# Performance work log

Measured on AMD Instinct MI355X. Metric: run time of the kernel, lower is better.

Reference implementation:

```python
import jax, jax.numpy as jnp
import numpy as np

NUM_QUANTIZERS = 8  # num_quantizes in __init__


def l2norm(t, eps=1e-12):
    return t / jnp.clip(jnp.linalg.norm(t, axis=-1, keepdims=True), eps)


def setup_inputs() -> dict:
    key = jax.random.key(0)
    k1, k2 = jax.random.split(key)
    x = jax.random.normal(k1, (1, 16384, 512), dtype=jnp.float32)
    codebook = jax.random.normal(k2, (2048, 512), dtype=jnp.float32)
    return {"x": x, "codebook": codebook}


def reference(x, codebook):
    # cosine-sim codebook: codes live on the unit sphere
    cb = l2norm(codebook)  # [K, D]

    def step(residual, _):
        rn = l2norm(residual)                       # [1, S, D]
        sim = jnp.einsum('bsd,kd->bsk', rn, cb)     # [1, S, K]
        idx = jnp.argmax(sim, axis=-1)              # [1, S]
        q = cb[idx]                                 # [1, S, D] gather
        # commit loss: mse(quantize.detach(), input)
        commit = jnp.mean((jax.lax.stop_gradient(q) - residual) ** 2)
        # straight-through estimator
        q_st = residual + jax.lax.stop_gradient(q - residual)
        return residual - q_st, (q_st, idx, commit)

    _, (quantized, indices, commits) = jax.lax.scan(
        step, x, None, length=NUM_QUANTIZERS)
    # quantized: [n, 1, S, D]; sum over quantizer axis (keepdim batch=1)
    quantized_sum = jnp.sum(quantized, axis=0)      # [1, S, D]
    all_indices = jnp.transpose(indices, (1, 2, 0))  # [1, S, n]
    commit_losses = commits[None, :]                # [1, n]
    return quantized_sum, all_indices, commit_losses
```

## Files before the change

### kernel.cpp

```cpp
#include <hip/hip_runtime.h>
#include <math.h>


#define TOKENS 16384
#define DDIM   512
#define NCODE  2048
#define NQ     8
#define CHUNK  4096

#define CBN_OFF  0u
#define G_OFF    1048576u
#define S_OFF    5242880u
#define ACC_FULL (S_OFF + (size_t)TOKENS * NCODE)
#define ACC_CHNK (S_OFF + (size_t)CHUNK  * NCODE)

#define QS_OFF   0u
#define IDX_OFF  8388608u
#define CL_OFF   8519680u

__global__ __launch_bounds__(256) void normalize_cb(const float* __restrict__ cb,
                                                    float* __restrict__ cbn,
                                                    float* __restrict__ acc) {
  if (blockIdx.x == 0 && threadIdx.x < NQ) acc[threadIdx.x] = 0.0f;
  int lane = threadIdx.x & 63;
  int wv   = threadIdx.x >> 6;
  int row  = blockIdx.x * 4 + wv;
  const float4* rp = (const float4*)(cb + (size_t)row * DDIM);
  float4 a = rp[lane * 2 + 0];
  float4 b = rp[lane * 2 + 1];
  float ss = a.x*a.x + a.y*a.y + a.z*a.z + a.w*a.w
           + b.x*b.x + b.y*b.y + b.z*b.z + b.w*b.w;
  #pragma unroll
  for (int o = 1; o < 64; o <<= 1) ss += __shfl_xor(ss, o);
  float nrm = fmaxf(sqrtf(ss), 1e-12f);
  float4 o0 = make_float4(a.x/nrm, a.y/nrm, a.z/nrm, a.w/nrm);
  float4 o1 = make_float4(b.x/nrm, b.y/nrm, b.z/nrm, b.w/nrm);
  float4* op = (float4*)(cbn + (size_t)row * DDIM);
  op[lane * 2 + 0] = o0;
  op[lane * 2 + 1] = o1;
}

__global__ void finalize(const float* __restrict__ acc, float* __restrict__ out) {
  if (threadIdx.x < NQ)
    out[CL_OFF + threadIdx.x] = acc[threadIdx.x] * (1.0f / ((float)TOKENS * (float)DDIM));
}

__global__ __launch_bounds__(256) void gemm_nt(const float* __restrict__ A,
                                               const float* __restrict__ B,
                                               float* __restrict__ C) {
  const int K = DDIM, N = NCODE;
  __shared__ float As[2][16][132];
  __shared__ float Bs[2][16][132];
  const int bn = blockIdx.x * 128;
  const int bm = blockIdx.y * 128;
  const int t  = threadIdx.x;
  const int tx = t & 15;
  const int ty = t >> 4;
  const int lr = t >> 2;
  const int lc = (t & 3) * 4;

  float acc[8][8];
  #pragma unroll
  for (int i = 0; i < 8; ++i)
    #pragma unroll
    for (int j = 0; j < 8; ++j) acc[i][j] = 0.0f;

  const float* Ap = A + (size_t)(bm + lr) * K + lc;
  const float* Bp = B + (size_t)(bn + lr) * K + lc;

  float4 a0 = *(const float4*)(Ap);
  float4 a1 = *(const float4*)(Ap + (size_t)64 * K);
  float4 b0 = *(const float4*)(Bp);
  float4 b1 = *(const float4*)(Bp + (size_t)64 * K);

  int cur = 0;
  for (int k0 = 0; k0 < K; k0 += 16) {
    As[cur][lc+0][lr]    = a0.x; As[cur][lc+1][lr]    = a0.y;
    As[cur][lc+2][lr]    = a0.z; As[cur][lc+3][lr]    = a0.w;
    As[cur][lc+0][lr+64] = a1.x; As[cur][lc+1][lr+64] = a1.y;
    As[cur][lc+2][lr+64] = a1.z; As[cur][lc+3][lr+64] = a1.w;
    Bs[cur][lc+0][lr]    = b0.x; Bs[cur][lc+1][lr]    = b0.y;
    Bs[cur][lc+2][lr]    = b0.z; Bs[cur][lc+3][lr]    = b0.w;
    Bs[cur][lc+0][lr+64] = b1.x; Bs[cur][lc+1][lr+64] = b1.y;
    Bs[cur][lc+2][lr+64] = b1.z; Bs[cur][lc+3][lr+64] = b1.w;
    if (k0 + 16 < K) {
      a0 = *(const float4*)(Ap + k0 + 16);
      a1 = *(const float4*)(Ap + (size_t)64 * K + k0 + 16);
      b0 = *(const float4*)(Bp + k0 + 16);
      b1 = *(const float4*)(Bp + (size_t)64 * K + k0 + 16);
    }
    __syncthreads();
    #pragma unroll
    for (int kk = 0; kk < 16; ++kk) {
      float av[8], bv[8];
      *(float4*)(av + 0) = *(const float4*)&As[cur][kk][ty * 4];
      *(float4*)(av + 4) = *(const float4*)&As[cur][kk][ty * 4 + 64];
      *(float4*)(bv + 0) = *(const float4*)&Bs[cur][kk][tx * 4];
      *(float4*)(bv + 4) = *(const float4*)&Bs[cur][kk][tx * 4 + 64];
      #pragma unroll
      for (int i = 0; i < 8; ++i)
        #pragma unroll
        for (int j = 0; j < 8; ++j) acc[i][j] += av[i] * bv[j];
    }
    cur ^= 1;
  }

  #pragma unroll
  for (int i = 0; i < 8; ++i) {
    int m = bm + ty * 4 + (i & 3) + ((i >> 2) << 6);
    float4 v0 = make_float4(acc[i][0], acc[i][1], acc[i][2], acc[i][3]);
    float4 v1 = make_float4(acc[i][4], acc[i][5], acc[i][6], acc[i][7]);
    *(float4*)&C[(size_t)m * N + bn + tx * 4]      = v0;
    *(float4*)&C[(size_t)m * N + bn + tx * 4 + 64] = v1;
  }
}

__global__ __launch_bounds__(256) void vq_steps(const float* __restrict__ S,
                                                const float* __restrict__ G,
                                                const float* __restrict__ cbn,
                                                const float* __restrict__ x,
                                                float* __restrict__ out,
                                                float* __restrict__ acc,
                                                int tok0) {
  const int lane = threadIdx.x & 63;
  const int wv   = threadIdx.x >> 6;
  const int trel = blockIdx.x * 4 + wv;
  const int tok  = tok0 + trel;

  float s[32];
  const float4* sp = (const float4*)(S + (size_t)trel * NCODE);
  #pragma unroll
  for (int q = 0; q < 8; ++q) {
    float4 v = sp[q * 64 + lane];
    s[q*4+0] = v.x; s[q*4+1] = v.y; s[q*4+2] = v.z; s[q*4+3] = v.w;
  }

  const float4* xp = (const float4*)(x + (size_t)tok * DDIM);
  float4 x0 = xp[lane * 2 + 0];
  float4 x1 = xp[lane * 2 + 1];
  float rho = x0.x*x0.x + x0.y*x0.y + x0.z*x0.z + x0.w*x0.w
            + x1.x*x1.x + x1.y*x1.y + x1.z*x1.z + x1.w*x1.w;
  #pragma unroll
  for (int o = 1; o < 64; o <<= 1) rho += __shfl_xor(rho, o);

  float qs[8] = {0.f,0.f,0.f,0.f,0.f,0.f,0.f,0.f};
  __shared__ float cl[4][NQ];

  for (int t = 0; t < NQ; ++t) {
    float tv[16]; int tc[16];
    #pragma unroll
    for (int r = 0; r < 16; ++r) {
      int ca = ((2*r) >> 2 << 8) + lane * 4 + ((2*r) & 3);
      float va = s[2*r], vb = s[2*r+1];
      bool b = vb > va;
      tv[r] = b ? vb : va;
      tc[r] = b ? ca + 1 : ca;
    }
    #pragma unroll
    for (int h = 8; h >= 1; h >>= 1) {
      #pragma unroll
      for (int r = 0; r < 16; ++r) {
        if (r < h) {
          bool b = tv[r + h] > tv[r];
          tv[r] = b ? tv[r + h] : tv[r];
          tc[r] = b ? tc[r + h] : tc[r];
        }
      }
    }
    float mv = tv[0];
    int   mc = tc[0];
    #pragma unroll
    for (int o = 1; o < 64; o <<= 1) {
      float ov = __shfl_xor(mv, o);
      int   oc = __shfl_xor(mc, o);
      if (ov > mv || (ov == mv && oc < mc)) { mv = ov; mc = oc; }
    }

    rho = rho - 2.0f * mv + 1.0f;
    if (lane == 0) {
      cl[wv][t] = rho;
      out[IDX_OFF + (size_t)tok * NQ + t] = (float)mc;
    }

    const float4* cr = (const float4*)(cbn + (size_t)mc * DDIM);
    float4 c0 = cr[lane * 2 + 0];
    float4 c1 = cr[lane * 2 + 1];
    qs[0]+=c0.x; qs[1]+=c0.y; qs[2]+=c0.z; qs[3]+=c0.w;
    qs[4]+=c1.x; qs[5]+=c1.y; qs[6]+=c1.z; qs[7]+=c1.w;

    if (t < NQ - 1) {
      const float4* gr = (const float4*)(G + (size_t)mc * NCODE);
      #pragma unroll
      for (int q = 0; q < 8; ++q) {
        float4 g = gr[q * 64 + lane];
        s[q*4+0] -= g.x; s[q*4+1] -= g.y; s[q*4+2] -= g.z; s[q*4+3] -= g.w;
      }
    }
  }

  float4* op = (float4*)(out + QS_OFF + (size_t)tok * DDIM);
  op[lane * 2 + 0] = make_float4(qs[0], qs[1], qs[2], qs[3]);
  op[lane * 2 + 1] = make_float4(qs[4], qs[5], qs[6], qs[7]);

  __syncthreads();
  if (threadIdx.x < NQ) {
    float v = cl[0][threadIdx.x] + cl[1][threadIdx.x]
            + cl[2][threadIdx.x] + cl[3][threadIdx.x];
    atomicAdd(&acc[threadIdx.x], v);
  }
}

extern "C" void kernel_launch(void* const* d_in, const int* in_sizes, int n_in,
                              void* d_out, int out_size, void* d_ws, size_t ws_size,
                              hipStream_t stream) {
  const float* x  = (const float*)d_in[0];
  const float* cb = (const float*)d_in[1];
  float* out = (float*)d_out;
  float* ws  = (float*)d_ws;

  float* cbn = ws + CBN_OFF;
  float* G   = ws + G_OFF;
  float* S   = ws + S_OFF;

  const size_t need_full = (ACC_FULL + 16) * sizeof(float);
  const bool full = ws_size >= need_full;
  float* acc = ws + (full ? ACC_FULL : ACC_CHNK);

  normalize_cb<<<NCODE / 4, 256, 0, stream>>>(cb, cbn, acc);
  gemm_nt<<<dim3(NCODE / 128, NCODE / 128), 256, 0, stream>>>(cbn, cbn, G);

  if (full) {
    gemm_nt<<<dim3(NCODE / 128, TOKENS / 128), 256, 0, stream>>>(x, cbn, S);
    vq_steps<<<TOKENS / 4, 256, 0, stream>>>(S, G, cbn, x, out, acc, 0);
  } else {
    for (int c = 0; c < TOKENS / CHUNK; ++c) {
      gemm_nt<<<dim3(NCODE / 128, CHUNK / 128), 256, 0, stream>>>(
          x + (size_t)c * CHUNK * DDIM, cbn, S);
      vq_steps<<<CHUNK / 4, 256, 0, stream>>>(S, G, cbn, x, out, acc, c * CHUNK);
    }
  }

  finalize<<<1, 64, 0, stream>>>(acc, out);
}
```

Measured before the change: 699.4 us.

## Compute token-code similarities with split-bf16 MFMA and exact near-tie rescoring

```diff
diff --git a/kernel.cpp b/kernel.cpp
--- a/kernel.cpp
+++ b/kernel.cpp
@@ -7,19 +7,40 @@
 #define NCODE  2048
 #define NQ     8
 #define CHUNK  4096
+#define DTHR   1e-3f
+
+typedef short   bf16x8  __attribute__((ext_vector_type(8)));
+typedef float   f32x4   __attribute__((ext_vector_type(4)));
+typedef short   s16x8   __attribute__((ext_vector_type(8)));
+
+#define GLOBAL_AS __attribute__((address_space(1)))
+#define LDS_AS    __attribute__((address_space(3)))
 
 #define CBN_OFF  0u
 #define G_OFF    1048576u
 #define S_OFF    5242880u
-#define ACC_FULL (S_OFF + (size_t)TOKENS * NCODE)
-#define ACC_CHNK (S_OFF + (size_t)CHUNK  * NCODE)
+#define XHI_OFF  13631488u
+#define XLO_OFF  17825792u
+#define BHI_OFF  22020096u
+#define BLO_OFF  22544384u
+#define ACC_OFF  23068672u
 
 #define QS_OFF   0u
 #define IDX_OFF  8388608u
 #define CL_OFF   8519680u
 
+__device__ inline unsigned short f2bf(float f) {
+  unsigned u = __float_as_uint(f);
+  return (unsigned short)((u + 0x7FFFu + ((u >> 16) & 1u)) >> 16);
+}
+__device__ inline float bf2f(unsigned short h) {
+  return __uint_as_float(((unsigned)h) << 16);
+}
+
 __global__ __launch_bounds__(256) void normalize_cb(const float* __restrict__ cb,
                                                     float* __restrict__ cbn,
+                                                    short* __restrict__ bhi,
+                                                    short* __restrict__ blo,
                                                     float* __restrict__ acc) {
   if (blockIdx.x == 0 && threadIdx.x < NQ) acc[threadIdx.x] = 0.0f;
   int lane = threadIdx.x & 63;
@@ -33,11 +54,45 @@
   #pragma unroll
   for (int o = 1; o < 64; o <<= 1) ss += __shfl_xor(ss, o);
   float nrm = fmaxf(sqrtf(ss), 1e-12f);
-  float4 o0 = make_float4(a.x/nrm, a.y/nrm, a.z/nrm, a.w/nrm);
-  float4 o1 = make_float4(b.x/nrm, b.y/nrm, b.z/nrm, b.w/nrm);
+  float v[8] = {a.x/nrm, a.y/nrm, a.z/nrm, a.w/nrm,
+                b.x/nrm, b.y/nrm, b.z/nrm, b.w/nrm};
   float4* op = (float4*)(cbn + (size_t)row * DDIM);
-  op[lane * 2 + 0] = o0;
-  op[lane * 2 + 1] = o1;
+  op[lane*2+0] = make_float4(v[0], v[1], v[2], v[3]);
+  op[lane*2+1] = make_float4(v[4], v[5], v[6], v[7]);
+
+  s16x8 h8, l8;
+  #pragma unroll
+  for (int i = 0; i < 8; ++i) {
+    unsigned short h = f2bf(v[i]);
+    h8[i] = (short)h;
+    l8[i] = (short)f2bf(v[i] - bf2f(h));
+  }
+  int nb = row >> 7, rr = row & 127, ks = lane >> 2, g = lane & 3;
+  size_t gidx = ((size_t)((nb * 16 + ks) * 4 + g) * 128 + rr) * 8;
+  *(s16x8*)(bhi + gidx) = h8;
+  *(s16x8*)(blo + gidx) = l8;
+}
+
+__global__ __launch_bounds__(256) void split_x(const float* __restrict__ x,
+                                               short* __restrict__ xhi,
+                                               short* __restrict__ xlo) {
+  int gid = blockIdx.x * 256 + threadIdx.x;
+  int r  = gid & 127;
+  int g  = (gid >> 7) & 3;
+  int ks = (gid >> 9) & 15;
+  int mb = gid >> 13;
+  const float4* src = (const float4*)(x + (size_t)(mb * 128 + r) * DDIM + ks * 32 + g * 8);
+  float4 v0 = src[0], v1 = src[1];
+  float v[8] = {v0.x, v0.y, v0.z, v0.w, v1.x, v1.y, v1.z, v1.w};
+  s16x8 h8, l8;
+  #pragma unroll
+  for (int i = 0; i < 8; ++i) {
+    unsigned short h = f2bf(v[i]);
+    h8[i] = (short)h;
+    l8[i] = (short)f2bf(v[i] - bf2f(h));
+  }
+  *(s16x8*)(xhi + (size_t)gid * 8) = h8;
+  *(s16x8*)(xlo + (size_t)gid * 8) = l8;
 }
 
 __global__ void finalize(const float* __restrict__ acc, float* __restrict__ out) {
@@ -115,6 +170,78 @@
   }
 }
 
+__global__ __launch_bounds__(256) void mfma_s(const short* __restrict__ xhi,
+                                              const short* __restrict__ xlo,
+                                              const short* __restrict__ bhi,
+                                              const short* __restrict__ blo,
+                                              float* __restrict__ S, int mb0) {
+  __shared__ short lds[2][4][4096];
+  const int l  = threadIdx.x & 63;
+  const int w  = threadIdx.x >> 6;
+  const int wm = w >> 1, wn = w & 1;
+  const int MB = mb0 + blockIdx.y;
+  const int NB = blockIdx.x;
+
+  const short* src = (w == 0) ? xhi : (w == 1) ? xlo : (w == 2) ? bhi : blo;
+  const size_t tb  = (size_t)(((w < 2 ? MB : NB) * 16)) * 4096;
+
+  f32x4 acc[4][4];
+  #pragma unroll
+  for (int i = 0; i < 4; ++i)
+    #pragma unroll
+    for (int j = 0; j < 4; ++j)
+      acc[i][j] = (f32x4){0.f, 0.f, 0.f, 0.f};
+
+  #define STAGE(buf, ks)                                                        \
+    {                                                                           \
+      const short* gsrc = src + tb + (size_t)(ks) * 4096 + l * 8;               \
+      short* ldst = &lds[buf][w][0];                                            \
+      _Pragma("unroll")                                                         \
+      for (int c = 0; c < 8; ++c)                                               \
+        __builtin_amdgcn_global_load_lds(                                       \
+            (GLOBAL_AS const unsigned int*)(gsrc + c * 512),                    \
+            (LDS_AS unsigned int*)(ldst + c * 512), 16, 0, 0);                  \
+    }
+
+  STAGE(0, 0);
+  const int g = l >> 4, c16 = l & 15;
+  for (int ks = 0; ks < 16; ++ks) {
+    const int cur = ks & 1;
+    __syncthreads();
+    if (ks < 15) STAGE(cur ^ 1, ks + 1);
+    bf16x8 ah[4], al[4], bh[4], bl[4];
+    #pragma unroll
+    for (int f = 0; f < 4; ++f) {
+      int ar = (g * 128 + (wm * 64 + f * 16 + c16)) * 8;
+      int br = (g * 128 + (wn * 64 + f * 16 + c16)) * 8;
+      ah[f] = *(const bf16x8*)&lds[cur][0][ar];
+      al[f] = *(const bf16x8*)&lds[cur][1][ar];
+      bh[f] = *(const bf16x8*)&lds[cur][2][br];
+      bl[f] = *(const bf16x8*)&lds[cur][3][br];
+    }
+    #pragma unroll
+    for (int fm = 0; fm < 4; ++fm)
+      #pragma unroll
+      for (int fn = 0; fn < 4; ++fn) {
+        acc[fm][fn] = __builtin_amdgcn_mfma_f32_16x16x32_bf16(ah[fm], bh[fn], acc[fm][fn], 0, 0, 0);
+        acc[fm][fn] = __builtin_amdgcn_mfma_f32_16x16x32_bf16(ah[fm], bl[fn], acc[fm][fn], 0, 0, 0);
+        acc[fm][fn] = __builtin_amdgcn_mfma_f32_16x16x32_bf16(al[fm], bh[fn], acc[fm][fn], 0, 0, 0);
+      }
+  }
+  #undef STAGE
+
+  #pragma unroll
+  for (int fm = 0; fm < 4; ++fm)
+    #pragma unroll
+    for (int fn = 0; fn < 4; ++fn)
+      #pragma unroll
+      for (int reg = 0; reg < 4; ++reg) {
+        int m = blockIdx.y * 128 + wm * 64 + fm * 16 + g * 4 + reg;
+        int n = NB * 128 + wn * 64 + fn * 16 + c16;
+        S[(size_t)m * NCODE + n] = acc[fm][fn][reg];
+      }
+}
+
 __global__ __launch_bounds__(256) void vq_steps(const float* __restrict__ S,
                                                 const float* __restrict__ G,
                                                 const float* __restrict__ cbn,
@@ -145,6 +272,7 @@
 
   float qs[8] = {0.f,0.f,0.f,0.f,0.f,0.f,0.f,0.f};
   __shared__ float cl[4][NQ];
+  int i0=0,i1=0,i2=0,i3=0,i4=0,i5=0,i6=0;
 
   for (int t = 0; t < NQ; ++t) {
     float tv[16]; int tc[16];
@@ -176,6 +304,49 @@
       if (ov > mv || (ov == mv && oc < mc)) { mv = ov; mc = oc; }
     }
 
+    int cloc = 0;
+    #pragma unroll
+    for (int r = 0; r < 32; ++r) cloc += (s[r] >= mv - DTHR) ? 1 : 0;
+    #pragma unroll
+    for (int o = 1; o < 64; o <<= 1) cloc += __shfl_xor(cloc, o);
+    if (cloc > 1) {
+      float bv = -3.4e38f; int bc = 0x7FFFFFFF; int seen = 0;
+      for (int r = 0; r < 32 && seen < 64; ++r) {
+        unsigned long long mask = __ballot(s[r] >= mv - DTHR);
+        while (mask && seen < 64) {
+          int L = __ffsll((unsigned long long)mask) - 1;
+          mask &= mask - 1;
+          int kc = ((r >> 2) << 8) + L * 4 + (r & 3);
+          if (lane == seen) {
+            float e = 0.f;
+            const float* xr = x + (size_t)tok * DDIM;
+            const float* cr = cbn + (size_t)kc * DDIM;
+            for (int k = 0; k < DDIM; ++k) e = fmaf(xr[k], cr[k], e);
+            if (t > 0) e -= G[(size_t)i0 * NCODE + kc];
+            if (t > 1) e -= G[(size_t)i1 * NCODE + kc];
+            if (t > 2) e -= G[(size_t)i2 * NCODE + kc];
+            if (t > 3) e -= G[(size_t)i3 * NCODE + kc];
+            if (t > 4) e -= G[(size_t)i4 * NCODE + kc];
+            if (t > 5) e -= G[(size_t)i5 * NCODE + kc];
+            if (t > 6) e -= G[(size_t)i6 * NCODE + kc];
+            bv = e; bc = kc;
+          }
+          ++seen;
+        }
+      }
+      #pragma unroll
+      for (int o = 1; o < 64; o <<= 1) {
+        float ov = __shfl_xor(bv, o);
+        int   oc = __shfl_xor(bc, o);
+        if (ov > bv || (ov == bv && oc < bc)) { bv = ov; bc = oc; }
+      }
+      mv = bv; mc = bc;
+    }
+
+    if (t == 0) i0 = mc; else if (t == 1) i1 = mc; else if (t == 2) i2 = mc;
+    else if (t == 3) i3 = mc; else if (t == 4) i4 = mc; else if (t == 5) i5 = mc;
+    else if (t == 6) i6 = mc;
+
     rho = rho - 2.0f * mv + 1.0f;
     if (lane == 0) {
       cl[wv][t] = rho;
@@ -192,8 +363,8 @@
       const float4* gr = (const float4*)(G + (size_t)mc * NCODE);
       #pragma unroll
       for (int q = 0; q < 8; ++q) {
-        float4 g = gr[q * 64 + lane];
-        s[q*4+0] -= g.x; s[q*4+1] -= g.y; s[q*4+2] -= g.z; s[q*4+3] -= g.w;
+        float4 gv = gr[q * 64 + lane];
+        s[q*4+0] -= gv.x; s[q*4+1] -= gv.y; s[q*4+2] -= gv.z; s[q*4+3] -= gv.w;
       }
     }
   }
@@ -221,23 +392,20 @@
   float* cbn = ws + CBN_OFF;
   float* G   = ws + G_OFF;
   float* S   = ws + S_OFF;
-
-  const size_t need_full = (ACC_FULL + 16) * sizeof(float);
-  const bool full = ws_size >= need_full;
-  float* acc = ws + (full ? ACC_FULL : ACC_CHNK);
-
-  normalize_cb<<<NCODE / 4, 256, 0, stream>>>(cb, cbn, acc);
+  short* xhi = (short*)(ws + XHI_OFF);
+  short* xlo = (short*)(ws + XLO_OFF);
+  short* bhi = (short*)(ws + BHI_OFF);
+  short* blo = (short*)(ws + BLO_OFF);
+  float* acc = ws + ACC_OFF;
+
+  normalize_cb<<<NCODE / 4, 256, 0, stream>>>(cb, cbn, bhi, blo, acc);
+  split_x<<<4096, 256, 0, stream>>>(x, xhi, xlo);
   gemm_nt<<<dim3(NCODE / 128, NCODE / 128), 256, 0, stream>>>(cbn, cbn, G);
 
-  if (full) {
-    gemm_nt<<<dim3(NCODE / 128, TOKENS / 128), 256, 0, stream>>>(x, cbn, S);
-    vq_steps<<<TOKENS / 4, 256, 0, stream>>>(S, G, cbn, x, out, acc, 0);
-  } else {
-    for (int c = 0; c < TOKENS / CHUNK; ++c) {
-      gemm_nt<<<dim3(NCODE / 128, CHUNK / 128), 256, 0, stream>>>(
-          x + (size_t)c * CHUNK * DDIM, cbn, S);
-      vq_steps<<<CHUNK / 4, 256, 0, stream>>>(S, G, cbn, x, out, acc, c * CHUNK);
-    }
+  for (int c = 0; c < TOKENS / CHUNK; ++c) {
+    mfma_s<<<dim3(NCODE / 128, CHUNK / 128), 256, 0, stream>>>(
+        xhi, xlo, bhi, blo, S, c * (CHUNK / 128));
+    vq_steps<<<CHUNK / 4, 256, 0, stream>>>(S, G, cbn, x, out, acc, c * CHUNK);
   }
 
   finalize<<<1, 64, 0, stream>>>(acc, out);
```

Measured after the change: 668.9 us. -4.4%, faster.
